# Kernel optimization log

Hardware: AMD Instinct MI355X
Metric: run time of the kernel (lower is better)

The kernel has to match this reference:

```python
import jax, jax.numpy as jnp
import numpy as np

N = 100_000      # nodes
E = 1_600_000    # edges (avg degree 16)
D_IN, D_H, D_OUT = 128, 128, 64


def setup_inputs() -> dict:
    key = jax.random.key(0)
    ks = jax.random.split(key, 6)
    x = jax.random.normal(ks[0], (N, D_IN), jnp.float32)
    edge_index = jax.random.randint(ks[1], (2, E), 0, N, dtype=jnp.int32)
    W1 = jax.random.normal(ks[2], (D_IN, D_H), jnp.float32) / np.sqrt(D_IN)
    b1 = jnp.zeros((D_H,), jnp.float32)
    W2 = jax.random.normal(ks[3], (D_H, D_OUT), jnp.float32) / np.sqrt(D_H)
    b2 = jnp.zeros((D_OUT,), jnp.float32)
    return {"x": x, "edge_index": edge_index, "W1": W1, "b1": b1, "W2": W2, "b2": b2}


def _gcn_layer(x, W, b, src, dst, n_nodes):
    # PyG GCNConv: h = x @ W; symmetric norm with self-loops; scatter-add; + bias
    h = x @ W                                        # [N, D_out]
    deg = jax.ops.segment_sum(jnp.ones_like(dst, jnp.float32), dst,
                              num_segments=n_nodes)  # self-loops => deg >= 1
    dinv = jax.lax.rsqrt(deg)                        # deg^{-1/2}
    norm = dinv[src] * dinv[dst]                     # [E+N]
    msg = h[src] * norm[:, None]                     # gather + scale
    out = jax.ops.segment_sum(msg, dst, num_segments=n_nodes)  # scatter-add
    return out + b


def reference(x, edge_index, W1, b1, W2, b2):
    n = x.shape[0]
    loop = jnp.arange(n, dtype=edge_index.dtype)
    src = jnp.concatenate([edge_index[0], loop])     # add self-loops
    dst = jnp.concatenate([edge_index[1], loop])
    h = _gcn_layer(x, W1, b1, src, dst, n)
    h = jax.nn.relu(h)
    # dropout(p=0.5) is identity in eval mode
    out = _gcn_layer(h, W2, b2, src, dst, n)
    return out
```

## Files before the change

### kernel.cpp

```cpp
#include <hip/hip_runtime.h>
#include <hip/hip_bf16.h>


#define NTHREADS 256
#define BSH 9
#define NBMAX 256

typedef unsigned int uint;
typedef unsigned short ushort;
typedef __attribute__((ext_vector_type(8))) short short8;
typedef __attribute__((ext_vector_type(4))) float floatx4;

__device__ __forceinline__ uint pack_bf16(float a, float b) {
    __hip_bfloat162 h = __float22bfloat162_rn(make_float2(a, b));
    return *reinterpret_cast<uint*>(&h);
}
__device__ __forceinline__ float bf16_lo(uint q) { return __uint_as_float(q << 16); }
__device__ __forceinline__ float bf16_hi(uint q) { return __uint_as_float(q & 0xffff0000u); }
__device__ __forceinline__ float bf16_one(ushort u) { return __uint_as_float(((uint)u) << 16); }

__global__ __launch_bounds__(256) void bucket_hist_kernel(
    const int* __restrict__ dst, int* __restrict__ bcnt, int e, int nb) {
    __shared__ int hist[NBMAX];
    int t = threadIdx.x;
    for (int b = t; b < nb; b += 256) hist[b] = 0;
    __syncthreads();
    int e0 = blockIdx.x * 2048;
#pragma unroll
    for (int i = 0; i < 8; i++) {
        int gi = e0 + t + i * 256;
        if (gi < e) atomicAdd(&hist[dst[gi] >> BSH], 1);
    }
    __syncthreads();
    for (int b = t; b < nb; b += 256) {
        int v = hist[b];
        if (v) atomicAdd(&bcnt[b], v);
    }
}

__global__ void bucket_scan(const int* __restrict__ bcnt, int* __restrict__ bstart,
                            int* __restrict__ bcursor, int nb) {
    __shared__ int buf[NBMAX];
    int t = threadIdx.x;
    int v = (t < nb) ? bcnt[t] : 0;
    buf[t] = v;
    __syncthreads();
    int x = v;
    for (int off = 1; off < NBMAX; off <<= 1) {
        int y = (t >= off) ? buf[t - off] : 0;
        __syncthreads();
        x += y;
        buf[t] = x;
        __syncthreads();
    }
    if (t < nb) {
        bstart[t] = x - v;
        bcursor[t] = x - v;
    }
}

__global__ __launch_bounds__(256) void partition_kernel(
    const int* __restrict__ src, const int* __restrict__ dst,
    int* __restrict__ bcursor, int2* __restrict__ staged, int e, int nb) {
    __shared__ int eS[2048];
    __shared__ int eD[2048];
    __shared__ int hist[NBMAX];
    __shared__ int base[NBMAX];
    int t = threadIdx.x;
    int e0 = blockIdx.x * 2048;

    for (int b = t; b < nb; b += 256) hist[b] = 0;
    __syncthreads();
#pragma unroll
    for (int i = 0; i < 8; i++) {
        int li = t + i * 256;
        int gi = e0 + li;
        int s = 0, d = -1;
        if (gi < e) { s = src[gi]; d = dst[gi]; }
        eS[li] = s;
        eD[li] = d;
        if (d >= 0) atomicAdd(&hist[d >> BSH], 1);
    }
    __syncthreads();
    for (int b = t; b < nb; b += 256) {
        int v = hist[b];
        base[b] = v ? atomicAdd(&bcursor[b], v) : 0;
        hist[b] = 0;
    }
    __syncthreads();
#pragma unroll
    for (int i = 0; i < 8; i++) {
        int li = t + i * 256;
        int d = eD[li];
        if (d >= 0) {
            int b = d >> BSH;
            int r = atomicAdd(&hist[b], 1);
            staged[base[b] + r] = make_int2(eS[li], d);
        }
    }
}

__global__ __launch_bounds__(256) void fine_count_kernel(
    const int2* __restrict__ staged, const int* __restrict__ bstart,
    const int* __restrict__ bcnt, int* __restrict__ cnt,
    int* __restrict__ startA, float* __restrict__ dinv, int n) {
    __shared__ int lcnt[512];
    __shared__ int tsum[256];
    int b = blockIdx.x;
    int t = threadIdx.x;
    lcnt[t] = 0;
    lcnt[t + 256] = 0;
    __syncthreads();
    int s0 = bstart[b];
    int m = bcnt[b];
    for (int i = t; i < m; i += 256)
        atomicAdd(&lcnt[staged[s0 + i].y & 511], 1);
    __syncthreads();
    int v0 = lcnt[2 * t];
    int v1 = lcnt[2 * t + 1];
    int tot = v0 + v1;
    tsum[t] = tot;
    __syncthreads();
    int x = tot;
    for (int off = 1; off < 256; off <<= 1) {
        int y = (t >= off) ? tsum[t - off] : 0;
        __syncthreads();
        x += y;
        tsum[t] = x;
        __syncthreads();
    }
    int excl = x - tot;
    int node = (b << BSH) + 2 * t;
    if (node < n) {
        cnt[node] = v0;
        startA[node] = s0 + excl;
        dinv[node] = rsqrtf((float)v0 + 1.0f);
    }
    if (node + 1 < n) {
        cnt[node + 1] = v1;
        startA[node + 1] = s0 + excl + v0;
        dinv[node + 1] = rsqrtf((float)v1 + 1.0f);
    }
}

__global__ __launch_bounds__(256) void fine_fill_kernel(
    const int2* __restrict__ staged, const int* __restrict__ bstart,
    const int* __restrict__ bcnt, const int* __restrict__ startA,
    const float* __restrict__ dinv, int2* __restrict__ rec, int n) {
    __shared__ int lcur[512];
    __shared__ float ldv[512];
    int b = blockIdx.x;
    int t = threadIdx.x;
    int nb0 = b << BSH;
    for (int i = t; i < 512; i += 256) {
        int node = nb0 + i;
        lcur[i] = (node < n) ? startA[node] : 0;
        ldv[i] = (node < n) ? dinv[node] : 0.f;
    }
    __syncthreads();
    int s0 = bstart[b];
    int m = bcnt[b];
    for (int i = t; i < m; i += 256) {
        int2 ed = staged[s0 + i];
        int li = ed.y & 511;
        int pos = atomicAdd(&lcur[li], 1);
        float nw = dinv[ed.x] * ldv[li];
        rec[pos] = make_int2(ed.x, __float_as_int(nw));
    }
}

template <int COLS, bool XF32>
__global__ __launch_bounds__(256) void gemm_mfma(const void* __restrict__ Xv,
                                                 const float* __restrict__ W,
                                                 uint* __restrict__ Cq, int n) {
    __shared__ ushort sX[64 * 128];
    __shared__ ushort sWT[COLS * 128];
    int t = threadIdx.x;
    int rbase = blockIdx.x * 64;

    if (XF32) {
        const float* X = (const float*)Xv;
#pragma unroll
        for (int i = 0; i < 8; i++) {
            int f = t + 256 * i;
            int r = f >> 5;
            int c4 = f & 31;
            float4 v = make_float4(0.f, 0.f, 0.f, 0.f);
            int gr = rbase + r;
            if (gr < n) v = *(const float4*)(X + (size_t)gr * 128 + c4 * 4);
            uint lo = pack_bf16(v.x, v.y);
            uint hi = pack_bf16(v.z, v.w);
            int chunk = c4 >> 1;
            int sub = (c4 & 1) * 4;
            int off = r * 128 + (((chunk ^ (r & 15)) << 3) + sub);
            *(uint2*)&sX[off] = make_uint2(lo, hi);
        }
    } else {
        const ushort* X = (const ushort*)Xv;
#pragma unroll
        for (int i = 0; i < 4; i++) {
            int f = t + 256 * i;
            int r = f >> 4;
            int chunk = f & 15;
            uint4 v = make_uint4(0, 0, 0, 0);
            int gr = rbase + r;
            if (gr < n) v = *(const uint4*)(X + (size_t)gr * 128 + chunk * 8);
            int off = r * 128 + ((chunk ^ (r & 15)) << 3);
            *(uint4*)&sX[off] = v;
        }
    }
    {
        constexpr int UNITS = 64 * (COLS / 4);
        constexpr int PER_T = UNITS / 256;
#pragma unroll
        for (int i = 0; i < PER_T; i++) {
            int u = t + 256 * i;
            int kp = u / (COLS / 4);
            int n4 = u % (COLS / 4);
            int k = kp * 2;
            float4 w0 = *(const float4*)(W + (size_t)k * COLS + n4 * 4);
            float4 w1 = *(const float4*)(W + (size_t)(k + 1) * COLS + n4 * 4);
            int chunk = k >> 3;
            int sub = k & 7;
            const float* a0 = (const float*)&w0;
            const float* a1 = (const float*)&w1;
#pragma unroll
            for (int j = 0; j < 4; j++) {
                int nn = n4 * 4 + j;
                uint pk = pack_bf16(a0[j], a1[j]);
                int off = nn * 128 + (((chunk ^ (nn & 15)) << 3) + sub);
                *(uint*)&sWT[off] = pk;
            }
        }
    }
    __syncthreads();

    int lane = t & 63;
    int wave = t >> 6;
    int m = lane & 15;
    int q = lane >> 4;
    int r0 = wave * 16;

    floatx4 acc[COLS / 16];
#pragma unroll
    for (int c = 0; c < COLS / 16; c++) acc[c] = (floatx4){0.f, 0.f, 0.f, 0.f};

#pragma unroll
    for (int ks = 0; ks < 4; ks++) {
        int rr = r0 + m;
        int ca = (ks * 4 + q) ^ (rr & 15);
        short8 afrag = *(const short8*)&sX[rr * 128 + (ca << 3)];
#pragma unroll
        for (int c = 0; c < COLS / 16; c++) {
            int nn = c * 16 + m;
            int cb = (ks * 4 + q) ^ (nn & 15);
            short8 bfrag = *(const short8*)&sWT[nn * 128 + (cb << 3)];
            acc[c] = __builtin_amdgcn_mfma_f32_16x16x32_bf16(bfrag, afrag, acc[c], 0, 0, 0);
        }
    }

    int gr = rbase + r0 + m;
    if (gr < n) {
#pragma unroll
        for (int c = 0; c < COLS / 16; c++) {
            uint2 pk;
            pk.x = pack_bf16(acc[c][0], acc[c][1]);
            pk.y = pack_bf16(acc[c][2], acc[c][3]);
            *(uint2*)&Cq[(size_t)gr * (COLS / 2) + c * 8 + q * 2] = pk;
        }
    }
}

__global__ __launch_bounds__(256) void aggregate128q(
    const uint* __restrict__ hq, const int2* __restrict__ rec,
    const int* __restrict__ start, const int* __restrict__ cnt,
    const float* __restrict__ dinv, const float* __restrict__ bias,
    uint* __restrict__ outq, int n) {
    int w0 = (int)((blockIdx.x * blockDim.x + threadIdx.x) >> 6);
    int w = __builtin_amdgcn_readfirstlane(w0);
    if (w >= n) return;
    int lane = threadIdx.x & 63;

    float di = dinv[w];
    float sw = di * di;
    uint qs = hq[(size_t)w * 64 + lane];
    float accx = bf16_lo(qs) * sw;
    float accy = bf16_hi(qs) * sw;

    int j0 = start[w];
    int deg = cnt[w];
    for (int base = 0; base < deg; base += 64) {
        int m = min(64, deg - base);
        int2 r = make_int2(0, 0);
        if (lane < m) r = rec[j0 + base + lane];
        int t = 0;
        for (; t + 8 <= m; t += 8) {
            int s[8];
            float wf[8];
            uint q[8];
#pragma unroll
            for (int u = 0; u < 8; u++) {
                s[u] = __shfl(r.x, t + u);
                wf[u] = __int_as_float(__shfl(r.y, t + u));
            }
#pragma unroll
            for (int u = 0; u < 8; u++) q[u] = hq[(size_t)s[u] * 64 + lane];
#pragma unroll
            for (int u = 0; u < 8; u++) {
                accx += bf16_lo(q[u]) * wf[u];
                accy += bf16_hi(q[u]) * wf[u];
            }
        }
        for (; t + 4 <= m; t += 4) {
            int s0 = __shfl(r.x, t + 0), s1 = __shfl(r.x, t + 1);
            int s2 = __shfl(r.x, t + 2), s3 = __shfl(r.x, t + 3);
            float w0f = __int_as_float(__shfl(r.y, t + 0));
            float w1f = __int_as_float(__shfl(r.y, t + 1));
            float w2f = __int_as_float(__shfl(r.y, t + 2));
            float w3f = __int_as_float(__shfl(r.y, t + 3));
            uint q0 = hq[(size_t)s0 * 64 + lane];
            uint q1 = hq[(size_t)s1 * 64 + lane];
            uint q2 = hq[(size_t)s2 * 64 + lane];
            uint q3 = hq[(size_t)s3 * 64 + lane];
            accx += bf16_lo(q0) * w0f; accy += bf16_hi(q0) * w0f;
            accx += bf16_lo(q1) * w1f; accy += bf16_hi(q1) * w1f;
            accx += bf16_lo(q2) * w2f; accy += bf16_hi(q2) * w2f;
            accx += bf16_lo(q3) * w3f; accy += bf16_hi(q3) * w3f;
        }
        for (; t < m; t++) {
            int s = __shfl(r.x, t);
            float nw = __int_as_float(__shfl(r.y, t));
            uint q = hq[(size_t)s * 64 + lane];
            accx += bf16_lo(q) * nw;
            accy += bf16_hi(q) * nw;
        }
    }

    float ox = fmaxf(accx + bias[lane * 2], 0.f);
    float oy = fmaxf(accy + bias[lane * 2 + 1], 0.f);
    outq[(size_t)w * 64 + lane] = pack_bf16(ox, oy);
}

__global__ __launch_bounds__(256) void aggregate64q(
    const ushort* __restrict__ hq, const int2* __restrict__ rec,
    const int* __restrict__ start, const int* __restrict__ cnt,
    const float* __restrict__ dinv, const float* __restrict__ bias,
    float* __restrict__ out, int n) {
    int w0 = (int)((blockIdx.x * blockDim.x + threadIdx.x) >> 6);
    int w = __builtin_amdgcn_readfirstlane(w0);
    if (w >= n) return;
    int lane = threadIdx.x & 63;

    float di = dinv[w];
    float acc = bf16_one(hq[(size_t)w * 64 + lane]) * di * di;

    int j0 = start[w];
    int deg = cnt[w];
    for (int base = 0; base < deg; base += 64) {
        int m = min(64, deg - base);
        int2 r = make_int2(0, 0);
        if (lane < m) r = rec[j0 + base + lane];
        int t = 0;
        for (; t + 8 <= m; t += 8) {
            int s[8];
            float wf[8];
            float v[8];
#pragma unroll
            for (int u = 0; u < 8; u++) {
                s[u] = __shfl(r.x, t + u);
                wf[u] = __int_as_float(__shfl(r.y, t + u));
            }
#pragma unroll
            for (int u = 0; u < 8; u++) v[u] = bf16_one(hq[(size_t)s[u] * 64 + lane]);
#pragma unroll
            for (int u = 0; u < 8; u++) acc += v[u] * wf[u];
        }
        for (; t + 4 <= m; t += 4) {
            int s0 = __shfl(r.x, t + 0), s1 = __shfl(r.x, t + 1);
            int s2 = __shfl(r.x, t + 2), s3 = __shfl(r.x, t + 3);
            float w0f = __int_as_float(__shfl(r.y, t + 0));
            float w1f = __int_as_float(__shfl(r.y, t + 1));
            float w2f = __int_as_float(__shfl(r.y, t + 2));
            float w3f = __int_as_float(__shfl(r.y, t + 3));
            float v0 = bf16_one(hq[(size_t)s0 * 64 + lane]);
            float v1 = bf16_one(hq[(size_t)s1 * 64 + lane]);
            float v2 = bf16_one(hq[(size_t)s2 * 64 + lane]);
            float v3 = bf16_one(hq[(size_t)s3 * 64 + lane]);
            acc += v0 * w0f + v1 * w1f + v2 * w2f + v3 * w3f;
        }
        for (; t < m; t++) {
            int s = __shfl(r.x, t);
            float nw = __int_as_float(__shfl(r.y, t));
            acc += bf16_one(hq[(size_t)s * 64 + lane]) * nw;
        }
    }

    acc += bias[lane];
    out[(size_t)w * 64 + lane] = acc;
}

extern "C" void kernel_launch(void* const* d_in, const int* in_sizes, int n_in,
                              void* d_out, int out_size, void* d_ws, size_t ws_size,
                              hipStream_t stream) {
    const float* x = (const float*)d_in[0];
    const int* edge = (const int*)d_in[1];
    const float* W1 = (const float*)d_in[2];
    const float* b1 = (const float*)d_in[3];
    const float* W2 = (const float*)d_in[4];
    const float* b2 = (const float*)d_in[5];

    const int N = in_sizes[0] / 128;
    const int E = in_sizes[1] / 2;
    const int* src = edge;
    const int* dst = edge + E;
    const int NB = (N + (1 << BSH) - 1) >> BSH;

    char* p = (char*)d_ws;
    int* cnt = (int*)p;       p += (size_t)N * 4;
    int* startA = (int*)p;    p += (size_t)N * 4;
    int* bcnt = (int*)p;      p += NBMAX * 4;
    int* bstart = (int*)p;    p += NBMAX * 4;
    int* bcursor = (int*)p;   p += NBMAX * 4;
    float* dinv = (float*)p;  p += (size_t)N * 4;
    int2* rec = (int2*)p;     p += (size_t)E * 8;
    uint* hq = (uint*)p;      p += (size_t)N * 64 * 4;
    uint* g = (uint*)p;       p += (size_t)N * 64 * 4;
    ushort* h2q = (ushort*)p; p += (size_t)N * 64 * 2;

    int2* staged = (int2*)g;

    float* out = (float*)d_out;
    const int eblocks = (E + 2047) / 2048;

    (void)hipMemsetAsync(bcnt, 0, NBMAX * 4, stream);
    bucket_hist_kernel<<<eblocks, 256, 0, stream>>>(dst, bcnt, E, NB);
    bucket_scan<<<1, NBMAX, 0, stream>>>(bcnt, bstart, bcursor, NB);
    partition_kernel<<<eblocks, 256, 0, stream>>>(src, dst, bcursor, staged, E, NB);
    fine_count_kernel<<<NB, 256, 0, stream>>>(staged, bstart, bcnt, cnt, startA, dinv, N);
    fine_fill_kernel<<<NB, 256, 0, stream>>>(staged, bstart, bcnt, startA, dinv, rec, N);

    const int gblocks = (N + 63) / 64;

    gemm_mfma<128, true><<<gblocks, 256, 0, stream>>>(x, W1, hq, N);
    aggregate128q<<<(N + 3) / 4, 256, 0, stream>>>(hq, rec, startA, cnt, dinv, b1, g, N);

    gemm_mfma<64, false><<<gblocks, 256, 0, stream>>>(g, W2, (uint*)h2q, N);
    aggregate64q<<<(N + 3) / 4, 256, 0, stream>>>(h2q, rec, startA, cnt, dinv, b2, out, N);
}
```

Measured before the change: 329.9 us.

## Split wavefront into half-waves processing two edges per step, vectorize edge loads

The aggregation kernels now split each 64-lane wavefront into two 32-lane halves. Each half handles alternate edges and loads wider per-lane chunks (8 bytes in layer 1, 4 bytes in layer 2), then the halves are combined with a cross-half shuffle. Edge records are read directly with uniform loads instead of staged through lane shuffles, and the histogram and partition kernels read src/dst as int4. The aim is to double the neighbor rows in flight per wave and cut shuffle overhead, at the cost of a final reduction and idle half-wave lanes during the epilogue.

```diff
diff --git a/kernel.cpp b/kernel.cpp
--- a/kernel.cpp
+++ b/kernel.cpp
@@ -17,7 +17,6 @@
 }
 __device__ __forceinline__ float bf16_lo(uint q) { return __uint_as_float(q << 16); }
 __device__ __forceinline__ float bf16_hi(uint q) { return __uint_as_float(q & 0xffff0000u); }
-__device__ __forceinline__ float bf16_one(ushort u) { return __uint_as_float(((uint)u) << 16); }
 
 __global__ __launch_bounds__(256) void bucket_hist_kernel(
     const int* __restrict__ dst, int* __restrict__ bcnt, int e, int nb) {
@@ -27,9 +26,18 @@
     __syncthreads();
     int e0 = blockIdx.x * 2048;
 #pragma unroll
-    for (int i = 0; i < 8; i++) {
-        int gi = e0 + t + i * 256;
-        if (gi < e) atomicAdd(&hist[dst[gi] >> BSH], 1);
+    for (int v = 0; v < 2; v++) {
+        int gi = e0 + t * 8 + v * 4;
+        if (gi + 3 < e) {
+            int4 d4 = *(const int4*)&dst[gi];
+            atomicAdd(&hist[d4.x >> BSH], 1);
+            atomicAdd(&hist[d4.y >> BSH], 1);
+            atomicAdd(&hist[d4.z >> BSH], 1);
+            atomicAdd(&hist[d4.w >> BSH], 1);
+        } else {
+            for (int j = 0; j < 4; j++)
+                if (gi + j < e) atomicAdd(&hist[dst[gi + j] >> BSH], 1);
+        }
     }
     __syncthreads();
     for (int b = t; b < nb; b += 256) {
@@ -72,14 +80,27 @@
     for (int b = t; b < nb; b += 256) hist[b] = 0;
     __syncthreads();
 #pragma unroll
-    for (int i = 0; i < 8; i++) {
-        int li = t + i * 256;
+    for (int v = 0; v < 2; v++) {
+        int li = t * 8 + v * 4;
         int gi = e0 + li;
-        int s = 0, d = -1;
-        if (gi < e) { s = src[gi]; d = dst[gi]; }
-        eS[li] = s;
-        eD[li] = d;
-        if (d >= 0) atomicAdd(&hist[d >> BSH], 1);
+        int4 s4, d4;
+        if (gi + 3 < e) {
+            s4 = *(const int4*)&src[gi];
+            d4 = *(const int4*)&dst[gi];
+        } else {
+            const int* sp = &src[gi];
+            const int* dp = &dst[gi];
+            s4.x = (gi + 0 < e) ? sp[0] : 0;  d4.x = (gi + 0 < e) ? dp[0] : -1;
+            s4.y = (gi + 1 < e) ? sp[1] : 0;  d4.y = (gi + 1 < e) ? dp[1] : -1;
+            s4.z = (gi + 2 < e) ? sp[2] : 0;  d4.z = (gi + 2 < e) ? dp[2] : -1;
+            s4.w = (gi + 3 < e) ? sp[3] : 0;  d4.w = (gi + 3 < e) ? dp[3] : -1;
+        }
+        *(int4*)&eS[li] = s4;
+        *(int4*)&eD[li] = d4;
+        if (d4.x >= 0) atomicAdd(&hist[d4.x >> BSH], 1);
+        if (d4.y >= 0) atomicAdd(&hist[d4.y >> BSH], 1);
+        if (d4.z >= 0) atomicAdd(&hist[d4.z >> BSH], 1);
+        if (d4.w >= 0) atomicAdd(&hist[d4.w >> BSH], 1);
     }
     __syncthreads();
     for (int b = t; b < nb; b += 256) {
@@ -276,69 +297,83 @@
     const int* __restrict__ start, const int* __restrict__ cnt,
     const float* __restrict__ dinv, const float* __restrict__ bias,
     uint* __restrict__ outq, int n) {
-    int w0 = (int)((blockIdx.x * blockDim.x + threadIdx.x) >> 6);
-    int w = __builtin_amdgcn_readfirstlane(w0);
+    int w = (int)((blockIdx.x * blockDim.x + threadIdx.x) >> 6);
     if (w >= n) return;
     int lane = threadIdx.x & 63;
-
+    int half = lane >> 5;
+    int fl = lane & 31;
+    const uint2* h2 = (const uint2*)hq;
+
+    float a0 = 0.f, a1 = 0.f, a2 = 0.f, a3 = 0.f;
     float di = dinv[w];
-    float sw = di * di;
-    uint qs = hq[(size_t)w * 64 + lane];
-    float accx = bf16_lo(qs) * sw;
-    float accy = bf16_hi(qs) * sw;
-
-    int j0 = start[w];
-    int deg = cnt[w];
-    for (int base = 0; base < deg; base += 64) {
-        int m = min(64, deg - base);
-        int2 r = make_int2(0, 0);
-        if (lane < m) r = rec[j0 + base + lane];
-        int t = 0;
-        for (; t + 8 <= m; t += 8) {
-            int s[8];
-            float wf[8];
-            uint q[8];
-#pragma unroll
-            for (int u = 0; u < 8; u++) {
-                s[u] = __shfl(r.x, t + u);
-                wf[u] = __int_as_float(__shfl(r.y, t + u));
-            }
-#pragma unroll
-            for (int u = 0; u < 8; u++) q[u] = hq[(size_t)s[u] * 64 + lane];
-#pragma unroll
-            for (int u = 0; u < 8; u++) {
-                accx += bf16_lo(q[u]) * wf[u];
-                accy += bf16_hi(q[u]) * wf[u];
-            }
-        }
-        for (; t + 4 <= m; t += 4) {
-            int s0 = __shfl(r.x, t + 0), s1 = __shfl(r.x, t + 1);
-            int s2 = __shfl(r.x, t + 2), s3 = __shfl(r.x, t + 3);
-            float w0f = __int_as_float(__shfl(r.y, t + 0));
-            float w1f = __int_as_float(__shfl(r.y, t + 1));
-            float w2f = __int_as_float(__shfl(r.y, t + 2));
-            float w3f = __int_as_float(__shfl(r.y, t + 3));
-            uint q0 = hq[(size_t)s0 * 64 + lane];
-            uint q1 = hq[(size_t)s1 * 64 + lane];
-            uint q2 = hq[(size_t)s2 * 64 + lane];
-            uint q3 = hq[(size_t)s3 * 64 + lane];
-            accx += bf16_lo(q0) * w0f; accy += bf16_hi(q0) * w0f;
-            accx += bf16_lo(q1) * w1f; accy += bf16_hi(q1) * w1f;
-            accx += bf16_lo(q2) * w2f; accy += bf16_hi(q2) * w2f;
-            accx += bf16_lo(q3) * w3f; accy += bf16_hi(q3) * w3f;
-        }
-        for (; t < m; t++) {
-            int s = __shfl(r.x, t);
-            float nw = __int_as_float(__shfl(r.y, t));
-            uint q = hq[(size_t)s * 64 + lane];
-            accx += bf16_lo(q) * nw;
-            accy += bf16_hi(q) * nw;
-        }
-    }
-
-    float ox = fmaxf(accx + bias[lane * 2], 0.f);
-    float oy = fmaxf(accy + bias[lane * 2 + 1], 0.f);
-    outq[(size_t)w * 64 + lane] = pack_bf16(ox, oy);
+    if (half == 0) {
+        uint2 q = h2[(size_t)w * 32 + fl];
+        float sw = di * di;
+        a0 = bf16_lo(q.x) * sw; a1 = bf16_hi(q.x) * sw;
+        a2 = bf16_lo(q.y) * sw; a3 = bf16_hi(q.y) * sw;
+    }
+    int j0 = __builtin_amdgcn_readfirstlane(start[w]);
+    int deg = __builtin_amdgcn_readfirstlane(cnt[w]);
+    const int2* rp = rec + j0;
+
+    int t = 0;
+    for (; t + 16 <= deg; t += 16) {
+        uint2 q[8]; float wf[8];
+#pragma unroll
+        for (int u = 0; u < 8; u++) {
+            int2 ea = rp[t + 2 * u];
+            int2 eb = rp[t + 2 * u + 1];
+            int s = half ? eb.x : ea.x;
+            wf[u] = __int_as_float(half ? eb.y : ea.y);
+            q[u] = h2[(size_t)s * 32 + fl];
+        }
+#pragma unroll
+        for (int u = 0; u < 8; u++) {
+            a0 += bf16_lo(q[u].x) * wf[u]; a1 += bf16_hi(q[u].x) * wf[u];
+            a2 += bf16_lo(q[u].y) * wf[u]; a3 += bf16_hi(q[u].y) * wf[u];
+        }
+    }
+    for (; t + 4 <= deg; t += 4) {
+        uint2 q[2]; float wf[2];
+#pragma unroll
+        for (int u = 0; u < 2; u++) {
+            int2 ea = rp[t + 2 * u];
+            int2 eb = rp[t + 2 * u + 1];
+            int s = half ? eb.x : ea.x;
+            wf[u] = __int_as_float(half ? eb.y : ea.y);
+            q[u] = h2[(size_t)s * 32 + fl];
+        }
+#pragma unroll
+        for (int u = 0; u < 2; u++) {
+            a0 += bf16_lo(q[u].x) * wf[u]; a1 += bf16_hi(q[u].x) * wf[u];
+            a2 += bf16_lo(q[u].y) * wf[u]; a3 += bf16_hi(q[u].y) * wf[u];
+        }
+    }
+    for (; t < deg; t += 2) {
+        int2 ea = rp[t];
+        int2 eb = (t + 1 < deg) ? rp[t + 1] : make_int2(0, 0);
+        int s = half ? eb.x : ea.x;
+        float wfv = __int_as_float(half ? eb.y : ea.y);
+        uint2 q = h2[(size_t)s * 32 + fl];
+        a0 += bf16_lo(q.x) * wfv; a1 += bf16_hi(q.x) * wfv;
+        a2 += bf16_lo(q.y) * wfv; a3 += bf16_hi(q.y) * wfv;
+    }
+
+    a0 += __shfl(a0, lane ^ 32);
+    a1 += __shfl(a1, lane ^ 32);
+    a2 += __shfl(a2, lane ^ 32);
+    a3 += __shfl(a3, lane ^ 32);
+    if (half == 0) {
+        float4 bb = *(const float4*)&bias[4 * fl];
+        float o0 = fmaxf(a0 + bb.x, 0.f);
+        float o1 = fmaxf(a1 + bb.y, 0.f);
+        float o2 = fmaxf(a2 + bb.z, 0.f);
+        float o3 = fmaxf(a3 + bb.w, 0.f);
+        uint2 pk;
+        pk.x = pack_bf16(o0, o1);
+        pk.y = pack_bf16(o2, o3);
+        *(uint2*)&outq[(size_t)w * 64 + fl * 2] = pk;
+    }
 }
 
 __global__ __launch_bounds__(256) void aggregate64q(
@@ -346,57 +381,77 @@
     const int* __restrict__ start, const int* __restrict__ cnt,
     const float* __restrict__ dinv, const float* __restrict__ bias,
     float* __restrict__ out, int n) {
-    int w0 = (int)((blockIdx.x * blockDim.x + threadIdx.x) >> 6);
-    int w = __builtin_amdgcn_readfirstlane(w0);
+    int w = (int)((blockIdx.x * blockDim.x + threadIdx.x) >> 6);
     if (w >= n) return;
     int lane = threadIdx.x & 63;
-
+    int half = lane >> 5;
+    int fl = lane & 31;
+    const uint* h2 = (const uint*)hq;
+
+    float a0 = 0.f, a1 = 0.f;
     float di = dinv[w];
-    float acc = bf16_one(hq[(size_t)w * 64 + lane]) * di * di;
-
-    int j0 = start[w];
-    int deg = cnt[w];
-    for (int base = 0; base < deg; base += 64) {
-        int m = min(64, deg - base);
-        int2 r = make_int2(0, 0);
-        if (lane < m) r = rec[j0 + base + lane];
-        int t = 0;
-        for (; t + 8 <= m; t += 8) {
-            int s[8];
-            float wf[8];
-            float v[8];
-#pragma unroll
-            for (int u = 0; u < 8; u++) {
-                s[u] = __shfl(r.x, t + u);
-                wf[u] = __int_as_float(__shfl(r.y, t + u));
-            }
-#pragma unroll
-            for (int u = 0; u < 8; u++) v[u] = bf16_one(hq[(size_t)s[u] * 64 + lane]);
-#pragma unroll
-            for (int u = 0; u < 8; u++) acc += v[u] * wf[u];
-        }
-        for (; t + 4 <= m; t += 4) {
-            int s0 = __shfl(r.x, t + 0), s1 = __shfl(r.x, t + 1);
-            int s2 = __shfl(r.x, t + 2), s3 = __shfl(r.x, t + 3);
-            float w0f = __int_as_float(__shfl(r.y, t + 0));
-            float w1f = __int_as_float(__shfl(r.y, t + 1));
-            float w2f = __int_as_float(__shfl(r.y, t + 2));
-            float w3f = __int_as_float(__shfl(r.y, t + 3));
-            float v0 = bf16_one(hq[(size_t)s0 * 64 + lane]);
-            float v1 = bf16_one(hq[(size_t)s1 * 64 + lane]);
-            float v2 = bf16_one(hq[(size_t)s2 * 64 + lane]);
-            float v3 = bf16_one(hq[(size_t)s3 * 64 + lane]);
-            acc += v0 * w0f + v1 * w1f + v2 * w2f + v3 * w3f;
-        }
-        for (; t < m; t++) {
-            int s = __shfl(r.x, t);
-            float nw = __int_as_float(__shfl(r.y, t));
-            acc += bf16_one(hq[(size_t)s * 64 + lane]) * nw;
-        }
-    }
-
-    acc += bias[lane];
-    out[(size_t)w * 64 + lane] = acc;
+    if (half == 0) {
+        uint q = h2[(size_t)w * 32 + fl];
+        float sw = di * di;
+        a0 = bf16_lo(q) * sw;
+        a1 = bf16_hi(q) * sw;
+    }
+    int j0 = __builtin_amdgcn_readfirstlane(start[w]);
+    int deg = __builtin_amdgcn_readfirstlane(cnt[w]);
+    const int2* rp = rec + j0;
+
+    int t = 0;
+    for (; t + 16 <= deg; t += 16) {
+        uint q[8]; float wf[8];
+#pragma unroll
+        for (int u = 0; u < 8; u++) {
+            int2 ea = rp[t + 2 * u];
+            int2 eb = rp[t + 2 * u + 1];
+            int s = half ? eb.x : ea.x;
+            wf[u] = __int_as_float(half ? eb.y : ea.y);
+            q[u] = h2[(size_t)s * 32 + fl];
+        }
+#pragma unroll
+        for (int u = 0; u < 8; u++) {
+            a0 += bf16_lo(q[u]) * wf[u];
+            a1 += bf16_hi(q[u]) * wf[u];
+        }
+    }
+    for (; t + 4 <= deg; t += 4) {
+        uint q[2]; float wf[2];
+#pragma unroll
+        for (int u = 0; u < 2; u++) {
+            int2 ea = rp[t + 2 * u];
+            int2 eb = rp[t + 2 * u + 1];
+            int s = half ? eb.x : ea.x;
+            wf[u] = __int_as_float(half ? eb.y : ea.y);
+            q[u] = h2[(size_t)s * 32 + fl];
+        }
+#pragma unroll
+        for (int u = 0; u < 2; u++) {
+            a0 += bf16_lo(q[u]) * wf[u];
+            a1 += bf16_hi(q[u]) * wf[u];
+        }
+    }
+    for (; t < deg; t += 2) {
+        int2 ea = rp[t];
+        int2 eb = (t + 1 < deg) ? rp[t + 1] : make_int2(0, 0);
+        int s = half ? eb.x : ea.x;
+        float wfv = __int_as_float(half ? eb.y : ea.y);
+        uint q = h2[(size_t)s * 32 + fl];
+        a0 += bf16_lo(q) * wfv;
+        a1 += bf16_hi(q) * wfv;
+    }
+
+    a0 += __shfl(a0, lane ^ 32);
+    a1 += __shfl(a1, lane ^ 32);
+    if (half == 0) {
+        float2 bb = *(const float2*)&bias[2 * fl];
+        float2 o;
+        o.x = a0 + bb.x;
+        o.y = a1 + bb.y;
+        ((float2*)out)[(size_t)w * 32 + fl] = o;
+    }
 }
 
 extern "C" void kernel_launch(void* const* d_in, const int* in_sizes, int n_in,
```

Result: no change. 323.6 us (-1.9%).
